# Performance work log

Hardware: AMD Instinct MI355X
Metric: run time of the kernel (lower is better)

The kernel has to match this reference:

```python
import jax, jax.numpy as jnp
import numpy as np

B, N, DQ, DK, DV = 8, 2048, 1024, 1024, 1024

def setup_inputs() -> dict:
    key = jax.random.key(0)
    kx, kq, kk, kv = jax.random.split(key, 4)
    x = jax.random.normal(kx, (B, N, DQ), dtype=jnp.float32)
    # nn.Linear(dim_q, dim_k, bias=False) weights: [out, in]
    s = 1.0 / np.sqrt(DQ)
    Wq = jax.random.uniform(kq, (DK, DQ), jnp.float32, -s, s)
    Wk = jax.random.uniform(kk, (DK, DQ), jnp.float32, -s, s)
    Wv = jax.random.uniform(kv, (DV, DQ), jnp.float32, -s, s)
    return {"x": x, "Wq": Wq, "Wk": Wk, "Wv": Wv}

def reference(x, Wq, Wk, Wv):
    batch, n, _ = x.shape
    q = jnp.einsum('bnd,kd->bnk', x, Wq)  # [B,n,DK]
    k = jnp.einsum('bnd,kd->bnk', x, Wk)  # [B,n,DK]
    v = jnp.einsum('bnd,vd->bnv', x, Wv)  # [B,n,DV]
    norm = 1.0 / jnp.sqrt(jnp.asarray(Wq.shape[0], jnp.float32))
    dist = jnp.einsum('bik,bjk->bij', q, k) * norm  # [B,n,n]
    causal = jnp.tril(jnp.ones((n, n), dtype=bool))
    dist = jnp.where(causal[None, :, :], dist, jnp.float32(-1e20))
    dist = jax.nn.softmax(dist, axis=-1)
    att = jnp.einsum('bij,bjv->biv', dist, v)  # [B,n,DV]
    return att
```

## Files before the change

### kernel.cpp

```cpp
#include <hip/hip_runtime.h>
#include <hip/hip_bf16.h>

#define BM 128
#define BN 128
#define BK 32
#define TILE_ELEMS (BM * BK)

typedef __attribute__((ext_vector_type(4))) float floatx4;
typedef __bf16 bf16x8 __attribute__((ext_vector_type(8)));
typedef unsigned int u32;
typedef unsigned short u16;

typedef __attribute__((address_space(1))) const u32 g_u32;
typedef __attribute__((address_space(3))) u32 l_u32;

__device__ __forceinline__ u16 f32_to_bf16(float f) {
    union { float f; u32 u; } x{f};
    u32 u = x.u;
    u32 r = (u + 0x7fffu + ((u >> 16) & 1u)) >> 16;
    return (u16)r;
}

__device__ __forceinline__ void stage_tile(const u16* gbase, int ld, u16* lds, int tid) {
#pragma unroll
    for (int it = 0; it < 2; ++it) {
        int flat = it * 2048 + tid * 8;
        int row = flat >> 5;
        int col = flat & 31;
        const u16* g = gbase + (long)row * ld + col;
        __builtin_amdgcn_global_load_lds((g_u32*)g, (l_u32*)(&lds[flat]), 16, 0, 0);
    }
}

template<bool OUT_BF16, int MODE>
__device__ __forceinline__ void gemm_body(
    const u16* __restrict__ Ab, const u16* __restrict__ Bb, void* __restrict__ Cb,
    int lda, int ldb, long ldc, int m0, int n0, int nkt, float scale,
    u16* As, u16* Bs, float* lsum)
{
    int tid = threadIdx.x;

    const u16* Arow = Ab + (long)m0 * lda;
    const u16* Brow = Bb + (long)n0 * ldb;

    stage_tile(Arow, lda, As, tid);
    stage_tile(Brow, ldb, Bs, tid);

    int wave = tid >> 6, lane = tid & 63;
    int wr = (wave >> 1) * 64, wc = (wave & 1) * 64;
    int lrow = lane & 15, quad = lane >> 4;

    floatx4 acc[4][4] = {};
    const int aoff = (wr + lrow) * BK + quad * 8;
    const int boff = (wc + lrow) * BK + quad * 8;

    for (int kt = 0; kt < nkt; ++kt) {
        __syncthreads();
        bf16x8 af[4], bfr[4];
#pragma unroll
        for (int i = 0; i < 4; ++i) {
            af[i]  = *(const bf16x8*)&As[aoff + i * 16 * BK];
            bfr[i] = *(const bf16x8*)&Bs[boff + i * 16 * BK];
        }
#pragma unroll
        for (int mi = 0; mi < 4; ++mi)
#pragma unroll
            for (int ni = 0; ni < 4; ++ni)
                acc[mi][ni] = __builtin_amdgcn_mfma_f32_16x16x32_bf16(af[mi], bfr[ni], acc[mi][ni], 0, 0, 0);
        __syncthreads();
        if (kt + 1 < nkt) {
            stage_tile(Arow + (kt + 1) * BK, lda, As, tid);
            stage_tile(Brow + (kt + 1) * BK, ldb, Bs, tid);
        }
    }

    long crow0 = m0 + wr + quad * 4;
    int  ccol0 = n0 + wc + lrow;
#pragma unroll
    for (int mi = 0; mi < 4; ++mi) {
#pragma unroll
        for (int r = 0; r < 4; ++r) {
            long row = crow0 + mi * 16 + r;
            float rs = 0.f;
            float linv = 1.f;
            if (MODE == 2) linv = 1.0f / lsum[row];
#pragma unroll
            for (int ni = 0; ni < 4; ++ni) {
                long col = ccol0 + ni * 16;
                float v = acc[mi][ni][r] * scale;
                if (MODE == 1) {
                    float e = (col > row) ? 0.f : __expf(v);
                    ((u16*)Cb)[row * ldc + col] = f32_to_bf16(e);
                    rs += e;
                } else if (MODE == 2) {
                    ((float*)Cb)[row * ldc + col] = v * linv;
                } else {
                    if (OUT_BF16) ((u16*)Cb)[row * ldc + col] = f32_to_bf16(v);
                    else          ((float*)Cb)[row * ldc + col] = v;
                }
            }
            if (MODE == 1) {
                rs += __shfl_xor(rs, 1, 16);
                rs += __shfl_xor(rs, 2, 16);
                rs += __shfl_xor(rs, 4, 16);
                rs += __shfl_xor(rs, 8, 16);
                if (lrow == 0) atomicAdd(&lsum[row], rs);
            }
        }
    }
}

__global__ __launch_bounds__(256)
void qkv_gemm(const u16* __restrict__ A, const u16* __restrict__ B, u16* __restrict__ C)
{
    __shared__ u16 As[TILE_ELEMS];
    __shared__ u16 Bs[TILE_ELEMS];
    int xcd = blockIdx.x, i = blockIdx.y;
    int mt = xcd * 16 + (i & 15);
    int nt = i >> 4;
    gemm_body<true, 0>(A, B, C, 1024, 1024, 3072,
                       mt * BM, nt * BN, 32, 1.0f, As, Bs, nullptr);
}

__global__ __launch_bounds__(256)
void s_gemm(const u16* __restrict__ QKVi, u16* __restrict__ P, float* __restrict__ lsum)
{
    __shared__ u16 As[TILE_ELEMS];
    __shared__ u16 Bs[TILE_ELEMS];
    int b = blockIdx.x, u = blockIdx.y, v = blockIdx.z;
    int mt, nt;
    if (u <= v) { mt = v; nt = u; } else { mt = 15 - v; nt = u - v - 1; }
    const u16* Ab = QKVi + (long)b * 2048 * 3072;
    const u16* Bb = Ab + 1024;
    gemm_body<true, 1>(Ab, Bb, P + (long)b * 2048 * 2048, 3072, 3072, 2048,
                       mt * BM, nt * BN, 32, 0.03125f, As, Bs, lsum + b * 2048);
}

__global__ __launch_bounds__(256)
void pv_gemm(const u16* __restrict__ P, const u16* __restrict__ Vt,
             float* __restrict__ O, const float* __restrict__ lsum)
{
    __shared__ u16 As[TILE_ELEMS];
    __shared__ u16 Bs[TILE_ELEMS];
    int b = blockIdx.x, nt = blockIdx.y, mt = blockIdx.z;
    const u16* Ab = P + (long)b * 2048 * 2048;
    const u16* Bb = Vt + (long)b * 2048;
    gemm_body<false, 2>(Ab, Bb, O + (long)b * 2048 * 1024, 2048, 16384, 1024,
                        mt * BM, nt * BN, mt * 4 + 4, 1.0f, As, Bs,
                        (float*)lsum + b * 2048);
}

__global__ __launch_bounds__(256)
void cvt_f32_bf16(const float* __restrict__ src, u16* __restrict__ dst, long n)
{
    long idx = ((long)blockIdx.x * 256 + threadIdx.x) << 2;
    if (idx >= n) return;
    float4 f = *(const float4*)(src + idx);
    ushort4 o;
    o.x = f32_to_bf16(f.x); o.y = f32_to_bf16(f.y);
    o.z = f32_to_bf16(f.z); o.w = f32_to_bf16(f.w);
    *(ushort4*)(dst + idx) = o;
}

__global__ __launch_bounds__(256)
void cvt_w3(const float* __restrict__ Wq, const float* __restrict__ Wk,
            const float* __restrict__ Wv, u16* __restrict__ dst)
{
    int which = blockIdx.x >> 10;
    const float* src = which == 0 ? Wq : (which == 1 ? Wk : Wv);
    long base = (long)(blockIdx.x & 1023) * 1024 + threadIdx.x * 4;
    float4 f = *(const float4*)(src + base);
    ushort4 o;
    o.x = f32_to_bf16(f.x); o.y = f32_to_bf16(f.y);
    o.z = f32_to_bf16(f.z); o.w = f32_to_bf16(f.w);
    *(ushort4*)(dst + (long)which * 1048576 + base) = o;
}

__global__ __launch_bounds__(256)
void transpose_v(const u16* __restrict__ QKVi, u16* __restrict__ Vt)
{
    __shared__ u16 tile[64][64 + 8];
    int t0 = blockIdx.x * 64;
    int d0 = blockIdx.y * 64;
    int tid = threadIdx.x;
    int lr = tid >> 3, lc = (tid & 7) * 8;
#pragma unroll
    for (int p = 0; p < 2; ++p) {
        int tok = lr + p * 32;
        const u16* src = QKVi + (long)(t0 + tok) * 3072 + 2048 + d0 + lc;
        *(uint4*)&tile[tok][lc] = *(const uint4*)src;
    }
    __syncthreads();
#pragma unroll
    for (int p = 0; p < 2; ++p) {
        int dq = lr + p * 32;
        u16 vals[8];
#pragma unroll
        for (int i = 0; i < 8; ++i) vals[i] = tile[lc + i][dq];
        *(uint4*)(Vt + (long)(d0 + dq) * 16384 + t0 + lc) = *(const uint4*)vals;
    }
}

extern "C" void kernel_launch(void* const* d_in, const int* in_sizes, int n_in,
                              void* d_out, int out_size, void* d_ws, size_t ws_size,
                              hipStream_t stream)
{
    const int B = 8, N = 2048, D = 1024;
    const long MT = (long)B * N;
    const long nX = MT * D;
    const long nW = (long)D * D;

    const float* x  = (const float*)d_in[0];
    const float* Wq = (const float*)d_in[1];
    const float* Wk = (const float*)d_in[2];
    const float* Wv = (const float*)d_in[3];
    float* out = (float*)d_out;

    u16* wb   = (u16*)d_ws;
    u16* xb   = wb + 3 * nW;
    u16* QKVi = xb + nX;
    u16* P    = QKVi + 3 * nX;
    u16* Vt   = xb;
    float* lsum = (float*)wb;

    cvt_f32_bf16<<<(int)(nX / 1024), 256, 0, stream>>>(x, xb, nX);
    cvt_w3<<<3072, 256, 0, stream>>>(Wq, Wk, Wv, wb);

    qkv_gemm<<<dim3(8, 384, 1), 256, 0, stream>>>(xb, wb, QKVi);

    hipMemsetAsync(lsum, 0, (size_t)B * N * sizeof(float), stream);
    transpose_v<<<dim3(256, 16, 1), 256, 0, stream>>>(QKVi, Vt);

    s_gemm<<<dim3(8, 17, 8), 256, 0, stream>>>(QKVi, P, lsum);

    pv_gemm<<<dim3(8, 8, 16), 256, 0, stream>>>(P, Vt, out, lsum);
}
```

Measured before the change: 411.1 us.

## Replace QKV projection GEMM with 256x256 double-buffered swizzled-LDS pipelined kernel

Rewrites the QKV projection GEMM to use 256x256 output tiles with 8 waves, BK=64 chunks and double-buffered LDS. Global-to-LDS loads are interleaved with the MFMA phases, with explicit vmcnt waits and barriers. An XOR-swizzled LDS layout is meant to avoid bank conflicts, and the tile order is remapped across XCDs. The aim is to hide memory latency and raise MFMA utilisation, at the cost of heavy LDS use (128KB) that limits occupancy.

Result: faster. 375.8 us (-8.6%).

```diff
diff --git a/kernel.cpp b/kernel.cpp
--- a/kernel.cpp
+++ b/kernel.cpp
@@ -20,6 +20,134 @@
     u32 r = (u + 0x7fffu + ((u >> 16) & 1u)) >> 16;
     return (u16)r;
 }
+
+
+__device__ __forceinline__ void stage_half_sw(const u16* gbase, u16* lds_half, int tid) {
+    int lane = tid & 63;
+    int rsub = lane >> 3;
+    int colsw = ((lane & 7) ^ rsub) << 3;
+#pragma unroll
+    for (int j = 0; j < 2; ++j) {
+        int q = (tid >> 6) * 2 + j;
+        int row = q * 8 + rsub;
+        const u16* g = gbase + row * 1024 + colsw;
+        u16* l = lds_half + q * 512 + lane * 8;
+        __builtin_amdgcn_global_load_lds((g_u32*)g, (l_u32*)l, 16, 0, 0);
+    }
+}
+
+__global__ __launch_bounds__(512, 2)
+void qkv_gemm8(const u16* __restrict__ A, const u16* __restrict__ Bw, u16* __restrict__ C)
+{
+    __shared__ u16 As[2][256 * 64];
+    __shared__ u16 Bs[2][256 * 64];
+
+    int bid = blockIdx.x;
+    int wg = (bid & 7) * 96 + (bid >> 3);
+    int mt = wg / 12, nt = wg - mt * 12;
+
+    int tid = threadIdx.x;
+    int lane = tid & 63, wv = tid >> 6;
+    int wr = wv >> 2, wc = wv & 3;
+    int lrow = lane & 15, quad = lane >> 4;
+    int sw = lrow & 7;
+
+    const u16* Ab = A + (long)mt * 256 * 1024;
+    const u16* Bb = Bw + (long)nt * 256 * 1024;
+
+    stage_half_sw(Bb,                  &Bs[0][0],        tid);
+    stage_half_sw(Bb + 128 * 1024,     &Bs[0][128 * 64], tid);
+    stage_half_sw(Ab,                  &As[0][0],        tid);
+    stage_half_sw(Ab + 128 * 1024,     &As[0][128 * 64], tid);
+    stage_half_sw(Bb + 64,             &Bs[1][0],        tid);
+    stage_half_sw(Bb + 64 + 128 * 1024,&Bs[1][128 * 64], tid);
+    asm volatile("s_waitcnt vmcnt(4)" ::: "memory");
+    __builtin_amdgcn_sched_barrier(0);
+    __builtin_amdgcn_s_barrier();
+
+    floatx4 acc[8][4] = {};
+
+    const int arow = (wr * 128 + lrow) * 64;
+    const int brow = (wc * 64 + lrow) * 64;
+    const int sl0 = (quad ^ sw) * 8;
+    const int sl1 = ((4 + quad) ^ sw) * 8;
+
+    for (int i = 0; i < 8; ++i) {
+        int t1  = 2 * i + 1;
+        int tn  = (2 * i + 2 <= 15) ? 2 * i + 2 : 15;
+        int tn1 = (2 * i + 3 <= 15) ? 2 * i + 3 : 15;
+        const u16* gA1 = Ab + t1 * 64;
+        const u16* gB2 = Bb + tn * 64;
+        const u16* gA2 = Ab + tn * 64;
+        const u16* gB3 = Bb + tn1 * 64;
+
+        bf16x8 bq0[4], bq1[4];
+#pragma unroll
+        for (int half = 0; half < 2; ++half) {
+#pragma unroll
+            for (int p = 0; p < 4; ++p) {
+                if (p == 0) {
+#pragma unroll
+                    for (int ni = 0; ni < 4; ++ni) {
+                        bq0[ni] = *(const bf16x8*)&Bs[half][brow + ni * 1024 + sl0];
+                        bq1[ni] = *(const bf16x8*)&Bs[half][brow + ni * 1024 + sl1];
+                    }
+                }
+                bf16x8 a00 = *(const bf16x8*)&As[half][arow + (2 * p)     * 1024 + sl0];
+                bf16x8 a01 = *(const bf16x8*)&As[half][arow + (2 * p)     * 1024 + sl1];
+                bf16x8 a10 = *(const bf16x8*)&As[half][arow + (2 * p + 1) * 1024 + sl0];
+                bf16x8 a11 = *(const bf16x8*)&As[half][arow + (2 * p + 1) * 1024 + sl1];
+
+                int ph = half * 4 + p;
+                switch (ph) {
+                    case 0: stage_half_sw(gA1,              &As[1][0],        tid); break;
+                    case 1: stage_half_sw(gA1 + 128 * 1024, &As[1][128 * 64], tid); break;
+                    case 2: stage_half_sw(gB2,              &Bs[0][0],        tid); break;
+                    case 3: stage_half_sw(gB2 + 128 * 1024, &Bs[0][128 * 64], tid); break;
+                    case 4: stage_half_sw(gA2,              &As[0][0],        tid); break;
+                    case 5: stage_half_sw(gA2 + 128 * 1024, &As[0][128 * 64], tid); break;
+                    case 6: stage_half_sw(gB3,              &Bs[1][0],        tid); break;
+                    case 7: stage_half_sw(gB3 + 128 * 1024, &Bs[1][128 * 64], tid); break;
+                }
+
+                __builtin_amdgcn_s_barrier();
+                __builtin_amdgcn_s_setprio(1);
+                int m0 = 2 * p;
+#pragma unroll
+                for (int ni = 0; ni < 4; ++ni) {
+                    acc[m0][ni]     = __builtin_amdgcn_mfma_f32_16x16x32_bf16(a00, bq0[ni], acc[m0][ni],     0, 0, 0);
+                    acc[m0][ni]     = __builtin_amdgcn_mfma_f32_16x16x32_bf16(a01, bq1[ni], acc[m0][ni],     0, 0, 0);
+                    acc[m0 + 1][ni] = __builtin_amdgcn_mfma_f32_16x16x32_bf16(a10, bq0[ni], acc[m0 + 1][ni], 0, 0, 0);
+                    acc[m0 + 1][ni] = __builtin_amdgcn_mfma_f32_16x16x32_bf16(a11, bq1[ni], acc[m0 + 1][ni], 0, 0, 0);
+                }
+                __builtin_amdgcn_s_setprio(0);
+                if (p == 3) {
+                    asm volatile("s_waitcnt vmcnt(4)" ::: "memory");
+                    __builtin_amdgcn_sched_barrier(0);
+                }
+                __builtin_amdgcn_s_barrier();
+            }
+        }
+    }
+    asm volatile("s_waitcnt vmcnt(0)" ::: "memory");
+    __builtin_amdgcn_sched_barrier(0);
+
+    long crow0 = (long)mt * 256 + wr * 128 + quad * 4;
+    int  ccol0 = nt * 256 + wc * 64 + lrow;
+#pragma unroll
+    for (int mi = 0; mi < 8; ++mi) {
+#pragma unroll
+        for (int r = 0; r < 4; ++r) {
+            long row = crow0 + mi * 16 + r;
+#pragma unroll
+            for (int ni = 0; ni < 4; ++ni) {
+                int col = ccol0 + ni * 16;
+                C[row * 3072 + col] = f32_to_bf16(acc[mi][ni][r]);
+            }
+        }
+    }
+}
+
 
 __device__ __forceinline__ void stage_tile(const u16* gbase, int ld, u16* lds, int tid) {
 #pragma unroll
@@ -111,18 +239,6 @@
 }
 
 __global__ __launch_bounds__(256)
-void qkv_gemm(const u16* __restrict__ A, const u16* __restrict__ B, u16* __restrict__ C)
-{
-    __shared__ u16 As[TILE_ELEMS];
-    __shared__ u16 Bs[TILE_ELEMS];
-    int xcd = blockIdx.x, i = blockIdx.y;
-    int mt = xcd * 16 + (i & 15);
-    int nt = i >> 4;
-    gemm_body<true, 0>(A, B, C, 1024, 1024, 3072,
-                       mt * BM, nt * BN, 32, 1.0f, As, Bs, nullptr);
-}
-
-__global__ __launch_bounds__(256)
 void s_gemm(const u16* __restrict__ QKVi, u16* __restrict__ P, float* __restrict__ lsum)
 {
     __shared__ u16 As[TILE_ELEMS];
@@ -226,7 +342,7 @@
     cvt_f32_bf16<<<(int)(nX / 1024), 256, 0, stream>>>(x, xb, nX);
     cvt_w3<<<3072, 256, 0, stream>>>(Wq, Wk, Wv, wb);
 
-    qkv_gemm<<<dim3(8, 384, 1), 256, 0, stream>>>(xb, wb, QKVi);
+    qkv_gemm8<<<dim3(768, 1, 1), 512, 0, stream>>>(xb, wb, QKVi);
 
     hipMemsetAsync(lsum, 0, (size_t)B * N * sizeof(float), stream);
     transpose_v<<<dim3(256, 16, 1), 256, 0, stream>>>(QKVi, Vt);
```
